# Optimization experiments

Hardware: AMD Instinct MI355X
Metric: run time of the kernel (lower is better)

## Reference

```python
import jax, jax.numpy as jnp
import numpy as np

B, S, H = 2, 1024, 2048
E, I, K = 32, 768, 4


def setup_inputs() -> dict:
    key = jax.random.key(0)
    k1, k2, k3, k4, k5 = jax.random.split(key, 5)
    sH = 1.0 / np.sqrt(H)
    sI = 1.0 / np.sqrt(I)
    return {
        "hidden_states": jax.random.normal(k1, (B, S, H), dtype=jnp.float32),
        "gate_w": jax.random.normal(k2, (E, H), dtype=jnp.float32) * sH,
        "w_gate": jax.random.normal(k3, (E, H, I), dtype=jnp.float32) * sH,
        "w_up": jax.random.normal(k4, (E, H, I), dtype=jnp.float32) * sH,
        "w_down": jax.random.normal(k5, (E, I, H), dtype=jnp.float32) * sI,
        "top_k": K,
    }


def reference(hidden_states, gate_w, w_gate, w_up, w_down, top_k):
    b, s, h = hidden_states.shape
    x = hidden_states.reshape(-1, h)                      # [T, H]
    T = x.shape[0]

    # Router: logits -> softmax over experts -> top-k -> renormalize
    logits = x @ gate_w.T                                 # [T, E]
    probs = jax.nn.softmax(logits, axis=-1)
    topv, topi = jax.lax.top_k(probs, top_k)              # [T, K]
    topv = topv / jnp.sum(topv, axis=-1, keepdims=True)   # norm_topk_prob

    # Dense routing-weight matrix (zero except selected experts) [T, E]
    rw = jnp.zeros((T, probs.shape[-1]), dtype=x.dtype)
    rw = rw.at[jnp.arange(T)[:, None], topi].set(topv)

    # Expert SwiGLU MLPs, computed for all experts then masked-combined
    g = jnp.einsum('th,ehi->eti', x, w_gate)              # [E, T, I]
    u = jnp.einsum('th,ehi->eti', x, w_up)                # [E, T, I]
    act = jax.nn.silu(g) * u                              # [E, T, I]
    expert_out = jnp.einsum('eti,eih->eth', act, w_down)  # [E, T, H]

    out = jnp.einsum('te,eth->th', rw, expert_out)        # combine [T, H]
    return out.reshape(b, s, h).astype(hidden_states.dtype)
```

## Files before the change

### kernel.cpp

```cpp
#include <hip/hip_runtime.h>
#include <hip/hip_bf16.h>
#include <math.h>

typedef unsigned short u16;
typedef unsigned int u32;
typedef short s16x8 __attribute__((ext_vector_type(8)));
typedef unsigned short u16x8 __attribute__((ext_vector_type(8)));
typedef float f32x4 __attribute__((ext_vector_type(4)));

#define TTOK 2048
#define HDIM 2048
#define ENUM 32
#define IDIM 768
#define KTOP 4

#define WS_XB   0L
#define WS_ACT  8388608L
#define WS_TIDX 20971520L
#define WS_TW   (WS_TIDX + 32768L)
#define WS_CNT  (WS_TW + 32768L)
#define WS_OFFS (WS_CNT + 128L)
#define WS_CUR  (WS_OFFS + 256L)
#define WS_RTOK (WS_CUR + 128L)
#define WS_RW   (WS_RTOK + 32768L)

#define LDA 40

__device__ __forceinline__ u16 f2bf(float f) {
  unsigned u = __builtin_bit_cast(unsigned, f);
  unsigned r = (u + 0x7fffu + ((u >> 16) & 1u)) >> 16;
  return (u16)r;
}
__device__ __forceinline__ unsigned pk2(float a, float b) {
  return (unsigned)f2bf(a) | ((unsigned)f2bf(b) << 16);
}

__global__ __launch_bounds__(256) void cvt_x_kernel(const float* __restrict__ x,
                                                    u16* __restrict__ xb) {
  long i = ((long)blockIdx.x * 256 + threadIdx.x) * 8;
  float4 a = *(const float4*)(x + i);
  float4 b = *(const float4*)(x + i + 4);
  uint4 o;
  o.x = pk2(a.x, a.y);
  o.y = pk2(a.z, a.w);
  o.z = pk2(b.x, b.y);
  o.w = pk2(b.z, b.w);
  *(uint4*)(xb + i) = o;
}

__global__ __launch_bounds__(256) void router_kernel(const float* __restrict__ x,
                                                     const float* __restrict__ gw,
                                                     int* __restrict__ tidx,
                                                     float* __restrict__ tw,
                                                     int* __restrict__ counts) {
  __shared__ float xs[HDIM];
  __shared__ float part[256];
  __shared__ float lg[ENUM];
  int t = blockIdx.x;
  const float4* xr = (const float4*)(x + (long)t * HDIM);
  float4* xs4 = (float4*)xs;
  for (int i = threadIdx.x; i < HDIM / 4; i += 256) xs4[i] = xr[i];
  __syncthreads();
  int e = threadIdx.x >> 3, ch = threadIdx.x & 7;
  const float4* gp = (const float4*)(gw + (long)e * HDIM + ch * 256);
  const float4* xp = (const float4*)(xs + ch * 256);
  float s = 0.f;
#pragma unroll 8
  for (int c = 0; c < 64; c++) {
    float4 gv = gp[c], xv = xp[c];
    s += gv.x * xv.x + gv.y * xv.y + gv.z * xv.z + gv.w * xv.w;
  }
  part[threadIdx.x] = s;
  __syncthreads();
  if (threadIdx.x < 32) {
    float v = 0.f;
#pragma unroll
    for (int j = 0; j < 8; j++) v += part[threadIdx.x * 8 + j];
    lg[threadIdx.x] = v;
  }
  __syncthreads();
  if (threadIdx.x == 0) {
    int sel[KTOP]; float sv[KTOP];
    unsigned mask = 0;
    for (int k = 0; k < KTOP; k++) {
      float best = -INFINITY; int bi = 0;
      for (int j = 0; j < ENUM; j++)
        if (!((mask >> j) & 1u) && lg[j] > best) { best = lg[j]; bi = j; }
      mask |= 1u << bi; sel[k] = bi; sv[k] = best;
    }
    float m = sv[0], den = 0.f, ex[KTOP];
    for (int k = 0; k < KTOP; k++) { ex[k] = expf(sv[k] - m); den += ex[k]; }
    for (int k = 0; k < KTOP; k++) {
      tidx[t * KTOP + k] = sel[k];
      tw[t * KTOP + k] = ex[k] / den;
      atomicAdd(&counts[sel[k]], 1);
    }
  }
}

__global__ void scan_kernel(const int* __restrict__ counts, int* __restrict__ offs,
                            int* __restrict__ cur) {
  if (threadIdx.x == 0) {
    int a = 0;
    for (int e = 0; e < ENUM; e++) { offs[e] = a; a += counts[e]; }
    offs[ENUM] = a;
  }
  if (threadIdx.x < ENUM) cur[threadIdx.x] = 0;
}

__global__ __launch_bounds__(256) void scatter_kernel(const int* __restrict__ tidx,
                                                      const float* __restrict__ tw,
                                                      const int* __restrict__ offs,
                                                      int* __restrict__ cur,
                                                      int* __restrict__ rtok,
                                                      float* __restrict__ rw) {
  int i = blockIdx.x * 256 + threadIdx.x;
  int e = tidx[i];
  int pos = atomicAdd(&cur[e], 1);
  int row = offs[e] + pos;
  rtok[row] = i >> 2;
  rw[row] = tw[i];
}

__global__ __launch_bounds__(512, 4) void gemm1_kernel(const u16* __restrict__ xb,
                                                       const float* __restrict__ wgp,
                                                       const float* __restrict__ wup,
                                                       const int* __restrict__ offs,
                                                       const int* __restrict__ rtok,
                                                       u16* __restrict__ act) {
  int d = blockIdx.x;
  int q8 = gridDim.x >> 3;
  int w = (d & 7) * q8 + (d >> 3);
  int nt = w % 12; int rem = w / 12; int mt = rem & 7; int e = rem >> 3;
  int off = offs[e], cnt = offs[e + 1] - off;
  int m0 = mt << 8;
  if (m0 >= cnt) return;
  int rows = cnt - m0; if (rows > 256) rows = 256;
  int baser = off + m0;
  int n0 = nt << 6;

  __shared__ __align__(16) u16 As[2][256 * LDA];
  __shared__ __align__(16) u16 Bsm[2][2][64 * LDA];

  int tid = threadIdx.x;
  int ln = tid & 63;
  int wv = tid >> 6;
  int wm = wv >> 1, wn = wv & 1;
  int lhi = ln >> 4;
  int llo = ln & 15;

  int ar = tid >> 1;
  int kcA = (tid & 1) * 16;
  int arow = ar < rows ? ar : rows - 1;
  const u16* aSrc = xb + (long)rtok[baser + arow] * HDIM + kcA;
  u16* aDst0 = &As[0][ar * LDA + kcA];
  u16* aDst1 = &As[1][ar * LDA + kcA];
  int half = tid >> 8;
  int t2 = tid & 255;
  int qk = t2 >> 4;
  int ncB = (t2 & 15) * 4;
  int qx = qk ^ ((t2 & 3) << 2);
  const float* bSrc = (half ? wup : wgp) + (long)e * (HDIM * IDIM) +
                      (long)(2 * qk) * IDIM + n0 + ncB;
  char* bDst0 = (char*)&Bsm[0][half][0] + qx * 4;
  char* bDst1 = (char*)&Bsm[1][half][0] + qx * 4;

  f32x4 accg[4][2], accu[4][2];
  f32x4 zz = {0.f, 0.f, 0.f, 0.f};
#pragma unroll
  for (int a = 0; a < 4; a++)
#pragma unroll
    for (int b = 0; b < 2; b++) { accg[a][b] = zz; accu[a][b] = zz; }

  u16x8 rA0, rA1;
  float4 rB0, rB1;

#define G1_LOAD(t)                                                   \
  {                                                                  \
    const u16* ap = aSrc + (t) * 32;                                 \
    rA0 = *(const u16x8*)ap;                                         \
    rA1 = *(const u16x8*)(ap + 8);                                   \
    const float* bp = bSrc + (long)(t) * 32 * IDIM;                  \
    rB0 = *(const float4*)bp;                                        \
    rB1 = *(const float4*)(bp + IDIM);                               \
  }
#define G1_WRITE(buf)                                                \
  {                                                                  \
    *(u16x8*)(buf ? aDst1 : aDst0) = rA0;                            \
    *(u16x8*)((buf ? aDst1 : aDst0) + 8) = rA1;                      \
    char* bd = buf ? bDst1 : bDst0;                                  \
    *(u32*)(bd + (ncB + 0) * 80) = pk2(rB0.x, rB1.x);                \
    *(u32*)(bd + (ncB + 1) * 80) = pk2(rB0.y, rB1.y);                \
    *(u32*)(bd + (ncB + 2) * 80) = pk2(rB0.z, rB1.z);                \
    *(u32*)(bd + (ncB + 3) * 80) = pk2(rB0.w, rB1.w);                \
  }

  const int NS = HDIM / 32;
  G1_LOAD(0);
  G1_WRITE(0);
  G1_LOAD(1);
  __syncthreads();

  for (int t = 0; t < NS; ++t) {
    int cur = t & 1;
    if (t + 1 < NS) G1_WRITE(cur ^ 1);
    if (t + 2 < NS) G1_LOAD(t + 2);
    {
      const u16* Ab = &As[cur][0];
      const u16* Bg = &Bsm[cur][0][0];
      const u16* Bu = &Bsm[cur][1][0];
      int g16 = lhi * 8;
      s16x8 a[4];
#pragma unroll
      for (int mf = 0; mf < 4; mf++) {
        int r = wm * 64 + mf * 16 + llo;
        a[mf] = *(const s16x8*)&Ab[r * LDA + g16];
      }
#pragma unroll
      for (int nf = 0; nf < 2; nf++) {
        int c = wn * 32 + nf * 16 + llo;
        int bo = c * LDA + ((lhi ^ ((c >> 2) & 3)) * 8);
        s16x8 bg = *(const s16x8*)&Bg[bo];
        s16x8 bu = *(const s16x8*)&Bu[bo];
#pragma unroll
        for (int mf = 0; mf < 4; mf++) {
          accg[mf][nf] = __builtin_amdgcn_mfma_f32_16x16x32_bf16(a[mf], bg, accg[mf][nf], 0, 0, 0);
          accu[mf][nf] = __builtin_amdgcn_mfma_f32_16x16x32_bf16(a[mf], bu, accu[mf][nf], 0, 0, 0);
        }
      }
    }
    __syncthreads();
  }

  int rbase = wm * 64 + lhi * 4;
  int cbase = n0 + wn * 32 + llo;
#pragma unroll
  for (int mf = 0; mf < 4; mf++) {
#pragma unroll
    for (int r4 = 0; r4 < 4; r4++) {
      int rl = rbase + mf * 16 + r4;
      if (rl < rows) {
        long rowb = (long)(baser + rl) * IDIM;
#pragma unroll
        for (int nf = 0; nf < 2; nf++) {
          float g = accg[mf][nf][r4], u = accu[mf][nf][r4];
          float av = g / (1.f + __expf(-g)) * u;
          act[rowb + cbase + nf * 16] = f2bf(av);
        }
      }
    }
  }
#undef G1_LOAD
#undef G1_WRITE
}

__global__ __launch_bounds__(512, 4) void gemm2_kernel(const u16* __restrict__ act,
                                                       const float* __restrict__ wdp,
                                                       const int* __restrict__ offs,
                                                       const int* __restrict__ rtok,
                                                       const float* __restrict__ rw,
                                                       float* __restrict__ out) {
  int d = blockIdx.x;
  int q8 = gridDim.x >> 3;
  int w = (d & 7) * q8 + (d >> 3);
  int nt = w & 15; int mt = (w >> 4) & 7; int e = w >> 7;
  int off = offs[e], cnt = offs[e + 1] - off;
  int m0 = mt << 8;
  if (m0 >= cnt) return;
  int rows = cnt - m0; if (rows > 256) rows = 256;
  int baser = off + m0;
  int n0 = nt << 7;

  __shared__ __align__(16) u16 As[2][256 * LDA];
  __shared__ __align__(16) u16 Bsm[2][128 * LDA];

  int tid = threadIdx.x;
  int ln = tid & 63;
  int wv = tid >> 6;
  int wm = wv >> 1, wn = wv & 1;
  int lhi = ln >> 4;
  int llo = ln & 15;

  int ar = tid >> 1;
  int kcA = (tid & 1) * 16;
  int arow = ar < rows ? ar : rows - 1;
  const u16* aSrc = act + (long)(baser + arow) * IDIM + kcA;
  u16* aDst0 = &As[0][ar * LDA + kcA];
  u16* aDst1 = &As[1][ar * LDA + kcA];

  int qk = tid >> 5;
  int ncB = (tid & 31) * 4;
  int qx = qk ^ ((tid & 3) << 2);
  const float* bSrc = wdp + (long)e * (IDIM * HDIM) + (long)(2 * qk) * HDIM + n0 + ncB;
  char* bDst0 = (char*)&Bsm[0][0] + qx * 4;
  char* bDst1 = (char*)&Bsm[1][0] + qx * 4;

  f32x4 acc[4][4];
  f32x4 zz = {0.f, 0.f, 0.f, 0.f};
#pragma unroll
  for (int a = 0; a < 4; a++)
#pragma unroll
    for (int b = 0; b < 4; b++) acc[a][b] = zz;

  u16x8 rA0, rA1;
  float4 rB0, rB1;

#define G2_LOAD(t)                                                   \
  {                                                                  \
    const u16* ap = aSrc + (t) * 32;                                 \
    rA0 = *(const u16x8*)ap;                                         \
    rA1 = *(const u16x8*)(ap + 8);                                   \
    const float* bp = bSrc + (long)(t) * 32 * HDIM;                  \
    rB0 = *(const float4*)bp;                                        \
    rB1 = *(const float4*)(bp + HDIM);                               \
  }
#define G2_WRITE(buf)                                                \
  {                                                                  \
    *(u16x8*)(buf ? aDst1 : aDst0) = rA0;                            \
    *(u16x8*)((buf ? aDst1 : aDst0) + 8) = rA1;                      \
    char* bd = buf ? bDst1 : bDst0;                                  \
    *(u32*)(bd + (ncB + 0) * 80) = pk2(rB0.x, rB1.x);                \
    *(u32*)(bd + (ncB + 1) * 80) = pk2(rB0.y, rB1.y);                \
    *(u32*)(bd + (ncB + 2) * 80) = pk2(rB0.z, rB1.z);                \
    *(u32*)(bd + (ncB + 3) * 80) = pk2(rB0.w, rB1.w);                \
  }

  const int NS = IDIM / 32;
  G2_LOAD(0);
  G2_WRITE(0);
  G2_LOAD(1);
  __syncthreads();

  for (int t = 0; t < NS; ++t) {
    int cur = t & 1;
    if (t + 1 < NS) G2_WRITE(cur ^ 1);
    if (t + 2 < NS) G2_LOAD(t + 2);
    {
      const u16* Ab = &As[cur][0];
      const u16* Bb = &Bsm[cur][0];
      int g16 = lhi * 8;
      s16x8 a[4];
#pragma unroll
      for (int mf = 0; mf < 4; mf++) {
        int r = wm * 64 + mf * 16 + llo;
        a[mf] = *(const s16x8*)&Ab[r * LDA + g16];
      }
#pragma unroll
      for (int nf = 0; nf < 4; nf++) {
        int c = wn * 64 + nf * 16 + llo;
        int bo = c * LDA + ((lhi ^ ((c >> 2) & 3)) * 8);
        s16x8 bv = *(const s16x8*)&Bb[bo];
#pragma unroll
        for (int mf = 0; mf < 4; mf++)
          acc[mf][nf] = __builtin_amdgcn_mfma_f32_16x16x32_bf16(a[mf], bv, acc[mf][nf], 0, 0, 0);
      }
    }
    __syncthreads();
  }

  int rbase = wm * 64 + lhi * 4;
  int cbase = n0 + wn * 64 + llo;
#pragma unroll
  for (int mf = 0; mf < 4; mf++) {
#pragma unroll
    for (int r4 = 0; r4 < 4; r4++) {
      int rl = rbase + mf * 16 + r4;
      if (rl < rows) {
        int rr = baser + rl;
        float wt = rw[rr];
        long ob = (long)rtok[rr] * HDIM + cbase;
#pragma unroll
        for (int nf = 0; nf < 4; nf++)
          atomicAdd(&out[ob + nf * 16], acc[mf][nf][r4] * wt);
      }
    }
  }
#undef G2_LOAD
#undef G2_WRITE
}

extern "C" void kernel_launch(void* const* d_in, const int* in_sizes, int n_in,
                              void* d_out, int out_size, void* d_ws, size_t ws_size,
                              hipStream_t stream) {
  const float* x = (const float*)d_in[0];
  const float* gw = (const float*)d_in[1];
  const float* wgate = (const float*)d_in[2];
  const float* wup = (const float*)d_in[3];
  const float* wdown = (const float*)d_in[4];
  float* out = (float*)d_out;

  char* ws = (char*)d_ws;
  u16* xb = (u16*)(ws + WS_XB);
  u16* act = (u16*)(ws + WS_ACT);
  int* tidx = (int*)(ws + WS_TIDX);
  float* tw = (float*)(ws + WS_TW);
  int* cnt = (int*)(ws + WS_CNT);
  int* offs = (int*)(ws + WS_OFFS);
  int* cur = (int*)(ws + WS_CUR);
  int* rtok = (int*)(ws + WS_RTOK);
  float* rw = (float*)(ws + WS_RW);

  hipMemsetAsync(cnt, 0, 128, stream);
  hipMemsetAsync(d_out, 0, (size_t)out_size * sizeof(float), stream);

  hipLaunchKernelGGL(cvt_x_kernel, dim3(TTOK * HDIM / (256 * 8)), dim3(256), 0, stream, x, xb);
  hipLaunchKernelGGL(router_kernel, dim3(TTOK), dim3(256), 0, stream, x, gw, tidx, tw, cnt);
  hipLaunchKernelGGL(scan_kernel, dim3(1), dim3(64), 0, stream, cnt, offs, cur);
  hipLaunchKernelGGL(scatter_kernel, dim3(TTOK * KTOP / 256), dim3(256), 0, stream, tidx, tw, offs, cur, rtok, rw);
  hipLaunchKernelGGL(gemm1_kernel, dim3(ENUM * 8 * 12), dim3(512), 0, stream, xb, wgate, wup, offs, rtok, act);
  hipLaunchKernelGGL(gemm2_kernel, dim3(ENUM * 8 * 16), dim3(512), 0, stream, act, wdown, offs, rtok, rw, out);
}
```

Baseline: 438.8 us.

## Halve GEMM N-tiles, use 8x1 warp layout and raise occupancy target

Both expert GEMMs switch to narrower output tiles: 32 columns in the gate/up GEMM and 64 in the down GEMM. Warps are now stacked 8x1 along M, and only part of the threads load and convert the fp32 weight tiles into LDS. This doubles the grid so that the few valid M-tiles per expert fill more CUs, and launch bounds are raised to allow more resident blocks. In exchange, activation rows are re-read from global memory twice as often, there is less MFMA work per LDS load, and the XOR swizzle on B stores is dropped, which may cause more LDS bank conflicts.

```diff
diff --git a/kernel.cpp b/kernel.cpp
--- a/kernel.cpp
+++ b/kernel.cpp
@@ -24,7 +24,7 @@
 #define WS_RTOK (WS_CUR + 128L)
 #define WS_RW   (WS_RTOK + 32768L)
 
-#define LDA 40
+#define LDAU 40
 
 __device__ __forceinline__ u16 f2bf(float f) {
   unsigned u = __builtin_bit_cast(unsigned, f);
@@ -122,7 +122,7 @@
   rw[row] = tw[i];
 }
 
-__global__ __launch_bounds__(512, 4) void gemm1_kernel(const u16* __restrict__ xb,
+__global__ __launch_bounds__(512, 6) void gemm1_kernel(const u16* __restrict__ xb,
                                                        const float* __restrict__ wgp,
                                                        const float* __restrict__ wup,
                                                        const int* __restrict__ offs,
@@ -131,44 +131,43 @@
   int d = blockIdx.x;
   int q8 = gridDim.x >> 3;
   int w = (d & 7) * q8 + (d >> 3);
-  int nt = w % 12; int rem = w / 12; int mt = rem & 7; int e = rem >> 3;
+  int nt = w % 24; int rem = w / 24; int mt = rem & 7; int e = rem >> 3;
   int off = offs[e], cnt = offs[e + 1] - off;
   int m0 = mt << 8;
   if (m0 >= cnt) return;
   int rows = cnt - m0; if (rows > 256) rows = 256;
   int baser = off + m0;
-  int n0 = nt << 6;
-
-  __shared__ __align__(16) u16 As[2][256 * LDA];
-  __shared__ __align__(16) u16 Bsm[2][2][64 * LDA];
+  int n0 = nt << 5;
+
+  __shared__ __align__(16) u16 As[2][256 * LDAU];
+  __shared__ __align__(16) u16 Bs[2][2][32 * LDAU];
 
   int tid = threadIdx.x;
   int ln = tid & 63;
   int wv = tid >> 6;
-  int wm = wv >> 1, wn = wv & 1;
-  int lhi = ln >> 4;
-  int llo = ln & 15;
+  int lhi = ln >> 4, llo = ln & 15;
 
   int ar = tid >> 1;
   int kcA = (tid & 1) * 16;
   int arow = ar < rows ? ar : rows - 1;
   const u16* aSrc = xb + (long)rtok[baser + arow] * HDIM + kcA;
-  u16* aDst0 = &As[0][ar * LDA + kcA];
-  u16* aDst1 = &As[1][ar * LDA + kcA];
-  int half = tid >> 8;
-  int t2 = tid & 255;
-  int qk = t2 >> 4;
-  int ncB = (t2 & 15) * 4;
-  int qx = qk ^ ((t2 & 3) << 2);
-  const float* bSrc = (half ? wup : wgp) + (long)e * (HDIM * IDIM) +
-                      (long)(2 * qk) * IDIM + n0 + ncB;
-  char* bDst0 = (char*)&Bsm[0][half][0] + qx * 4;
-  char* bDst1 = (char*)&Bsm[1][half][0] + qx * 4;
-
-  f32x4 accg[4][2], accu[4][2];
+  u16* aDst0 = &As[0][ar * LDAU + kcA];
+  u16* aDst1 = &As[1][ar * LDAU + kcA];
+
+  int isB = ((tid & 255) < 128);
+  int mat = tid >> 8;
+  int t2 = tid & 127;
+  int qk = t2 & 15;
+  int gg = t2 >> 4;
+  const float* bSrc = (mat ? wup : wgp) + (long)e * (HDIM * IDIM) +
+                      (long)(2 * qk) * IDIM + n0 + 4 * gg;
+  u16* bDst0 = &Bs[0][mat][4 * gg * LDAU + qk * 2];
+  u16* bDst1 = &Bs[1][mat][4 * gg * LDAU + qk * 2];
+
+  f32x4 accg[2][2], accu[2][2];
   f32x4 zz = {0.f, 0.f, 0.f, 0.f};
 #pragma unroll
-  for (int a = 0; a < 4; a++)
+  for (int a = 0; a < 2; a++)
 #pragma unroll
     for (int b = 0; b < 2; b++) { accg[a][b] = zz; accu[a][b] = zz; }
 
@@ -180,19 +179,24 @@
     const u16* ap = aSrc + (t) * 32;                                 \
     rA0 = *(const u16x8*)ap;                                         \
     rA1 = *(const u16x8*)(ap + 8);                                   \
-    const float* bp = bSrc + (long)(t) * 32 * IDIM;                  \
-    rB0 = *(const float4*)bp;                                        \
-    rB1 = *(const float4*)(bp + IDIM);                               \
+    if (isB) {                                                       \
+      const float* bp = bSrc + (long)(t) * 32 * IDIM;                \
+      rB0 = *(const float4*)bp;                                      \
+      rB1 = *(const float4*)(bp + IDIM);                             \
+    }                                                                \
   }
 #define G1_WRITE(buf)                                                \
   {                                                                  \
-    *(u16x8*)(buf ? aDst1 : aDst0) = rA0;                            \
-    *(u16x8*)((buf ? aDst1 : aDst0) + 8) = rA1;                      \
-    char* bd = buf ? bDst1 : bDst0;                                  \
-    *(u32*)(bd + (ncB + 0) * 80) = pk2(rB0.x, rB1.x);                \
-    *(u32*)(bd + (ncB + 1) * 80) = pk2(rB0.y, rB1.y);                \
-    *(u32*)(bd + (ncB + 2) * 80) = pk2(rB0.z, rB1.z);                \
-    *(u32*)(bd + (ncB + 3) * 80) = pk2(rB0.w, rB1.w);                \
+    u16* ad = buf ? aDst1 : aDst0;                                   \
+    *(u16x8*)ad = rA0;                                               \
+    *(u16x8*)(ad + 8) = rA1;                                         \
+    if (isB) {                                                       \
+      u16* bd = buf ? bDst1 : bDst0;                                 \
+      *(u32*)(bd + 0 * LDAU) = pk2(rB0.x, rB1.x);                    \
+      *(u32*)(bd + 1 * LDAU) = pk2(rB0.y, rB1.y);                    \
+      *(u32*)(bd + 2 * LDAU) = pk2(rB0.z, rB1.z);                    \
+      *(u32*)(bd + 3 * LDAU) = pk2(rB0.w, rB1.w);                    \
+    }                                                                \
   }
 
   const int NS = HDIM / 32;
@@ -206,24 +210,22 @@
     if (t + 1 < NS) G1_WRITE(cur ^ 1);
     if (t + 2 < NS) G1_LOAD(t + 2);
     {
-      const u16* Ab = &As[cur][0];
-      const u16* Bg = &Bsm[cur][0][0];
-      const u16* Bu = &Bsm[cur][1][0];
-      int g16 = lhi * 8;
-      s16x8 a[4];
-#pragma unroll
-      for (int mf = 0; mf < 4; mf++) {
-        int r = wm * 64 + mf * 16 + llo;
-        a[mf] = *(const s16x8*)&Ab[r * LDA + g16];
+      const u16* Ab = As[cur];
+      const u16* Bg = Bs[cur][0];
+      const u16* Bu = Bs[cur][1];
+      s16x8 a[2];
+#pragma unroll
+      for (int mf = 0; mf < 2; mf++) {
+        int r = wv * 32 + mf * 16 + llo;
+        a[mf] = *(const s16x8*)&Ab[r * LDAU + lhi * 8];
       }
 #pragma unroll
       for (int nf = 0; nf < 2; nf++) {
-        int c = wn * 32 + nf * 16 + llo;
-        int bo = c * LDA + ((lhi ^ ((c >> 2) & 3)) * 8);
-        s16x8 bg = *(const s16x8*)&Bg[bo];
-        s16x8 bu = *(const s16x8*)&Bu[bo];
-#pragma unroll
-        for (int mf = 0; mf < 4; mf++) {
+        int c = nf * 16 + llo;
+        s16x8 bg = *(const s16x8*)&Bg[c * LDAU + lhi * 8];
+        s16x8 bu = *(const s16x8*)&Bu[c * LDAU + lhi * 8];
+#pragma unroll
+        for (int mf = 0; mf < 2; mf++) {
           accg[mf][nf] = __builtin_amdgcn_mfma_f32_16x16x32_bf16(a[mf], bg, accg[mf][nf], 0, 0, 0);
           accu[mf][nf] = __builtin_amdgcn_mfma_f32_16x16x32_bf16(a[mf], bu, accu[mf][nf], 0, 0, 0);
         }
@@ -232,10 +234,10 @@
     __syncthreads();
   }
 
-  int rbase = wm * 64 + lhi * 4;
-  int cbase = n0 + wn * 32 + llo;
-#pragma unroll
-  for (int mf = 0; mf < 4; mf++) {
+  int rbase = wv * 32 + lhi * 4;
+  int cbase = n0 + llo;
+#pragma unroll
+  for (int mf = 0; mf < 2; mf++) {
 #pragma unroll
     for (int r4 = 0; r4 < 4; r4++) {
       int rl = rbase + mf * 16 + r4;
@@ -254,7 +256,7 @@
 #undef G1_WRITE
 }
 
-__global__ __launch_bounds__(512, 4) void gemm2_kernel(const u16* __restrict__ act,
+__global__ __launch_bounds__(512, 6) void gemm2_kernel(const u16* __restrict__ act,
                                                        const float* __restrict__ wdp,
                                                        const int* __restrict__ offs,
                                                        const int* __restrict__ rtok,
@@ -263,42 +265,40 @@
   int d = blockIdx.x;
   int q8 = gridDim.x >> 3;
   int w = (d & 7) * q8 + (d >> 3);
-  int nt = w & 15; int mt = (w >> 4) & 7; int e = w >> 7;
+  int nt = w & 31; int mt = (w >> 5) & 7; int e = w >> 8;
   int off = offs[e], cnt = offs[e + 1] - off;
   int m0 = mt << 8;
   if (m0 >= cnt) return;
   int rows = cnt - m0; if (rows > 256) rows = 256;
   int baser = off + m0;
-  int n0 = nt << 7;
-
-  __shared__ __align__(16) u16 As[2][256 * LDA];
-  __shared__ __align__(16) u16 Bsm[2][128 * LDA];
+  int n0 = nt << 6;
+
+  __shared__ __align__(16) u16 As[2][256 * LDAU];
+  __shared__ __align__(16) u16 Bs[2][64 * LDAU];
 
   int tid = threadIdx.x;
   int ln = tid & 63;
   int wv = tid >> 6;
-  int wm = wv >> 1, wn = wv & 1;
-  int lhi = ln >> 4;
-  int llo = ln & 15;
+  int lhi = ln >> 4, llo = ln & 15;
 
   int ar = tid >> 1;
   int kcA = (tid & 1) * 16;
   int arow = ar < rows ? ar : rows - 1;
   const u16* aSrc = act + (long)(baser + arow) * IDIM + kcA;
-  u16* aDst0 = &As[0][ar * LDA + kcA];
-  u16* aDst1 = &As[1][ar * LDA + kcA];
-
-  int qk = tid >> 5;
-  int ncB = (tid & 31) * 4;
-  int qx = qk ^ ((tid & 3) << 2);
-  const float* bSrc = wdp + (long)e * (IDIM * HDIM) + (long)(2 * qk) * HDIM + n0 + ncB;
-  char* bDst0 = (char*)&Bsm[0][0] + qx * 4;
-  char* bDst1 = (char*)&Bsm[1][0] + qx * 4;
-
-  f32x4 acc[4][4];
+  u16* aDst0 = &As[0][ar * LDAU + kcA];
+  u16* aDst1 = &As[1][ar * LDAU + kcA];
+
+  int isB = (tid < 256);
+  int qk = tid & 15;
+  int gg = (tid >> 4) & 15;
+  const float* bSrc = wdp + (long)e * (IDIM * HDIM) + (long)(2 * qk) * HDIM + n0 + 4 * gg;
+  u16* bDst0 = &Bs[0][4 * gg * LDAU + qk * 2];
+  u16* bDst1 = &Bs[1][4 * gg * LDAU + qk * 2];
+
+  f32x4 acc[2][4];
   f32x4 zz = {0.f, 0.f, 0.f, 0.f};
 #pragma unroll
-  for (int a = 0; a < 4; a++)
+  for (int a = 0; a < 2; a++)
 #pragma unroll
     for (int b = 0; b < 4; b++) acc[a][b] = zz;
 
@@ -310,19 +310,24 @@
     const u16* ap = aSrc + (t) * 32;                                 \
     rA0 = *(const u16x8*)ap;                                         \
     rA1 = *(const u16x8*)(ap + 8);                                   \
-    const float* bp = bSrc + (long)(t) * 32 * HDIM;                  \
-    rB0 = *(const float4*)bp;                                        \
-    rB1 = *(const float4*)(bp + HDIM);                               \
+    if (isB) {                                                       \
+      const float* bp = bSrc + (long)(t) * 32 * HDIM;                \
+      rB0 = *(const float4*)bp;                                      \
+      rB1 = *(const float4*)(bp + HDIM);                             \
+    }                                                                \
   }
 #define G2_WRITE(buf)                                                \
   {                                                                  \
-    *(u16x8*)(buf ? aDst1 : aDst0) = rA0;                            \
-    *(u16x8*)((buf ? aDst1 : aDst0) + 8) = rA1;                      \
-    char* bd = buf ? bDst1 : bDst0;                                  \
-    *(u32*)(bd + (ncB + 0) * 80) = pk2(rB0.x, rB1.x);                \
-    *(u32*)(bd + (ncB + 1) * 80) = pk2(rB0.y, rB1.y);                \
-    *(u32*)(bd + (ncB + 2) * 80) = pk2(rB0.z, rB1.z);                \
-    *(u32*)(bd + (ncB + 3) * 80) = pk2(rB0.w, rB1.w);                \
+    u16* ad = buf ? aDst1 : aDst0;                                   \
+    *(u16x8*)ad = rA0;                                               \
+    *(u16x8*)(ad + 8) = rA1;                                         \
+    if (isB) {                                                       \
+      u16* bd = buf ? bDst1 : bDst0;                                 \
+      *(u32*)(bd + 0 * LDAU) = pk2(rB0.x, rB1.x);                    \
+      *(u32*)(bd + 1 * LDAU) = pk2(rB0.y, rB1.y);                    \
+      *(u32*)(bd + 2 * LDAU) = pk2(rB0.z, rB1.z);                    \
+      *(u32*)(bd + 3 * LDAU) = pk2(rB0.w, rB1.w);                    \
+    }                                                                \
   }
 
   const int NS = IDIM / 32;
@@ -336,32 +341,30 @@
     if (t + 1 < NS) G2_WRITE(cur ^ 1);
     if (t + 2 < NS) G2_LOAD(t + 2);
     {
-      const u16* Ab = &As[cur][0];
-      const u16* Bb = &Bsm[cur][0];
-      int g16 = lhi * 8;
-      s16x8 a[4];
-#pragma unroll
-      for (int mf = 0; mf < 4; mf++) {
-        int r = wm * 64 + mf * 16 + llo;
-        a[mf] = *(const s16x8*)&Ab[r * LDA + g16];
+      const u16* Ab = As[cur];
+      const u16* Bb = Bs[cur];
+      s16x8 a[2];
+#pragma unroll
+      for (int mf = 0; mf < 2; mf++) {
+        int r = wv * 32 + mf * 16 + llo;
+        a[mf] = *(const s16x8*)&Ab[r * LDAU + lhi * 8];
       }
 #pragma unroll
       for (int nf = 0; nf < 4; nf++) {
-        int c = wn * 64 + nf * 16 + llo;
-        int bo = c * LDA + ((lhi ^ ((c >> 2) & 3)) * 8);
-        s16x8 bv = *(const s16x8*)&Bb[bo];
-#pragma unroll
-        for (int mf = 0; mf < 4; mf++)
+        int c = nf * 16 + llo;
+        s16x8 bv = *(const s16x8*)&Bb[c * LDAU + lhi * 8];
+#pragma unroll
+        for (int mf = 0; mf < 2; mf++)
           acc[mf][nf] = __builtin_amdgcn_mfma_f32_16x16x32_bf16(a[mf], bv, acc[mf][nf], 0, 0, 0);
       }
     }
     __syncthreads();
   }
 
-  int rbase = wm * 64 + lhi * 4;
-  int cbase = n0 + wn * 64 + llo;
-#pragma unroll
-  for (int mf = 0; mf < 4; mf++) {
+  int rbase = wv * 32 + lhi * 4;
+  int cbase = n0 + llo;
+#pragma unroll
+  for (int mf = 0; mf < 2; mf++) {
 #pragma unroll
     for (int r4 = 0; r4 < 4; r4++) {
       int rl = rbase + mf * 16 + r4;
@@ -407,6 +410,6 @@
   hipLaunchKernelGGL(router_kernel, dim3(TTOK), dim3(256), 0, stream, x, gw, tidx, tw, cnt);
   hipLaunchKernelGGL(scan_kernel, dim3(1), dim3(64), 0, stream, cnt, offs, cur);
   hipLaunchKernelGGL(scatter_kernel, dim3(TTOK * KTOP / 256), dim3(256), 0, stream, tidx, tw, offs, cur, rtok, rw);
-  hipLaunchKernelGGL(gemm1_kernel, dim3(ENUM * 8 * 12), dim3(512), 0, stream, xb, wgate, wup, offs, rtok, act);
-  hipLaunchKernelGGL(gemm2_kernel, dim3(ENUM * 8 * 16), dim3(512), 0, stream, act, wdown, offs, rtok, rw, out);
-}
+  hipLaunchKernelGGL(gemm1_kernel, dim3(ENUM * 8 * 24), dim3(512), 0, stream, xb, wgate, wup, offs, rtok, act);
+  hipLaunchKernelGGL(gemm2_kernel, dim3(ENUM * 8 * 32), dim3(512), 0, stream, act, wdown, offs, rtok, rw, out);
+}
```

Result: slower. 491.7 us (+12.0%).
